# Optimization experiments

Hardware: AMD Instinct MI355X
Metric: run time of the kernel (lower is better)

Reference implementation:

```python
import jax, jax.numpy as jnp
import numpy as np

B, L, D_MODEL = 4, 2048, 1024
D_STATE, D_CONV, EXPAND, HEADDIM = 128, 4, 2, 64
D_INNER = EXPAND * D_MODEL            # 2048
NHEADS = D_INNER // HEADDIM           # 32
CONV_DIM = D_INNER + 2 * D_STATE      # 2304
D_IN_PROJ = 2 * D_INNER + 2 * D_STATE + NHEADS  # 4448
EPS = 1e-5


def _silu(v):
    return v * jax.nn.sigmoid(v)


def setup_inputs() -> dict:
    key = jax.random.key(0)
    ks = jax.random.split(key, 8)
    x = jax.random.normal(ks[0], (B, L, D_MODEL), dtype=jnp.float32)
    ln_w = jnp.ones((D_MODEL,), jnp.float32)
    ln_b = jnp.zeros((D_MODEL,), jnp.float32)
    in_proj_w = jax.random.normal(ks[1], (D_IN_PROJ, D_MODEL), jnp.float32) * 0.02
    conv_w = jax.random.normal(ks[2], (CONV_DIM, D_CONV), jnp.float32) * 0.2
    conv_b = jnp.zeros((CONV_DIM,), jnp.float32)
    # inverse-softplus of dt sampled in [1e-3, 1e-1], matching mamba2 dt init
    dt_bias = jnp.log(jnp.expm1(jax.random.uniform(ks[3], (NHEADS,), minval=0.001, maxval=0.1)))
    # A sampled uniform in [1,16], stored as log (A = -exp(A_log))
    A_log = jnp.log(jax.random.uniform(ks[4], (NHEADS,), minval=1.0, maxval=16.0))
    D = jnp.ones((NHEADS,), jnp.float32)
    rms_w = jnp.ones((D_INNER,), jnp.float32)
    out_proj_w = jax.random.normal(ks[5], (D_MODEL, D_INNER), jnp.float32) * 0.02
    return {"x": x, "ln_w": ln_w, "ln_b": ln_b, "in_proj_w": in_proj_w,
            "conv_w": conv_w, "conv_b": conv_b, "dt_bias": dt_bias,
            "A_log": A_log, "D": D, "rms_w": rms_w, "out_proj_w": out_proj_w}


def reference(x, ln_w, ln_b, in_proj_w, conv_w, conv_b, dt_bias, A_log, D, rms_w, out_proj_w):
    b = x.shape[0]
    # LayerNorm
    mu = x.mean(-1, keepdims=True)
    var = ((x - mu) ** 2).mean(-1, keepdims=True)
    u = (x - mu) * jax.lax.rsqrt(var + EPS) * ln_w + ln_b
    # input projection -> z | xBC | dt
    zxbcdt = jnp.einsum('bld,ed->ble', u, in_proj_w)
    z = zxbcdt[..., :D_INNER]
    xBC = zxbcdt[..., D_INNER:D_INNER + CONV_DIM]
    dt = jax.nn.softplus(zxbcdt[..., -NHEADS:] + dt_bias)  # (b,l,h)
    # causal depthwise conv along time (kernel D_CONV) + silu
    xpad = jnp.pad(xBC, ((0, 0), (D_CONV - 1, 0), (0, 0)))
    conv = conv_b + sum(conv_w[:, k] * xpad[:, k:k + L, :] for k in range(D_CONV))
    xBC = _silu(conv)
    xh = xBC[..., :D_INNER].reshape(b, L, NHEADS, HEADDIM)       # (b,l,h,p)
    Bm = xBC[..., D_INNER:D_INNER + D_STATE]                      # (b,l,n)
    Cm = xBC[..., D_INNER + D_STATE:]                             # (b,l,n)
    A = -jnp.exp(A_log)                                           # (h,)
    dA = jnp.exp(dt * A)                                          # (b,l,h)
    dtx = dt[..., None] * xh                                      # (b,l,h,p)

    def step(h, inp):
        dA_t, dtx_t, B_t, C_t = inp
        h = dA_t[:, :, None, None] * h + dtx_t[..., None] * B_t[:, None, None, :]
        y_t = jnp.einsum('bhpn,bn->bhp', h, C_t)
        return h, y_t

    h0 = jnp.zeros((b, NHEADS, HEADDIM, D_STATE), x.dtype)
    xs = (dA.transpose(1, 0, 2), dtx.transpose(1, 0, 2, 3),
          Bm.transpose(1, 0, 2), Cm.transpose(1, 0, 2))
    _, ys = jax.lax.scan(step, h0, xs)                            # (l,b,h,p)
    y = ys.transpose(1, 0, 2, 3) + D[None, None, :, None] * xh    # skip term
    y = y.reshape(b, L, D_INNER)
    # gated RMSNorm: rmsnorm(y * silu(z)) * weight
    g = y * _silu(z)
    g = g * jax.lax.rsqrt((g * g).mean(-1, keepdims=True) + EPS) * rms_w
    out = jnp.einsum('ble,de->bld', g, out_proj_w)
    # residual; dropout is identity in eval mode
    return out + x
```

## Files before the change

### kernel.cpp

```cpp
#include <hip/hip_runtime.h>
#include <hip/hip_bf16.h>

#define DEV __device__ __forceinline__

typedef unsigned short u16;
typedef unsigned int u32;
typedef float f32x4 __attribute__((ext_vector_type(4)));
typedef short s16x8 __attribute__((ext_vector_type(8)));

static constexpr int Bb = 4, Ll = 2048, DM = 1024, DI = 2048, NH = 32;
static constexpr int CD = 2304;
static constexpr int NP = 4384;
static constexpr int NP_PAD = 4480;
static constexpr int BL = Bb * Ll;
static constexpr int NC = 32;

DEV float u2f(u16 s) { return __uint_as_float(((u32)s) << 16); }
DEV u16 f2bu(float f) {
  __hip_bfloat16 h = __float2bfloat16(f);
  u16 s; __builtin_memcpy(&s, &h, 2); return s;
}
DEV float blo(u32 u) { return __uint_as_float(u << 16); }
DEV float bhi(u32 u) { return __uint_as_float(u & 0xffff0000u); }

DEV int swz64(int r, int k)  { return r * 64  + ((((k >> 3) ^ (r & 7))) << 3) + (k & 7); }

DEV void gl_lds16(const u16* g, u16* l) {
  __builtin_amdgcn_global_load_lds(
      (const __attribute__((address_space(1))) u32*)g,
      (__attribute__((address_space(3))) u32*)l, 16, 0, 0);
}

__global__ __launch_bounds__(256) void cvt_pad(const float* __restrict__ src,
    u16* __restrict__ dst, int total, int cols, int realRows) {
  int i = blockIdx.x * 256 + threadIdx.x;
  if (i >= total) return;
  int r = i / cols;
  dst[i] = (r < realRows) ? f2bu(src[i]) : (u16)0;
}

__global__ __launch_bounds__(256) void ln_kernel(const float* __restrict__ x,
    const float* __restrict__ w, const float* __restrict__ bia, u16* __restrict__ u) {
  int row = blockIdx.x, tid = threadIdx.x;
  const float4* xr = (const float4*)(x + (size_t)row * DM);
  float4 v = xr[tid];
  float s = v.x + v.y + v.z + v.w;
  float s2 = v.x*v.x + v.y*v.y + v.z*v.z + v.w*v.w;
  #pragma unroll
  for (int o = 32; o; o >>= 1) { s += __shfl_down(s, o); s2 += __shfl_down(s2, o); }
  __shared__ float rs[4], rs2[4];
  int wv = tid >> 6, ln = tid & 63;
  if (ln == 0) { rs[wv] = s; rs2[wv] = s2; }
  __syncthreads();
  s = rs[0] + rs[1] + rs[2] + rs[3];
  s2 = rs2[0] + rs2[1] + rs2[2] + rs2[3];
  float mu = s * (1.f / DM);
  float var = s2 * (1.f / DM) - mu * mu;
  float inv = rsqrtf(var + 1e-5f);
  float4 wv4 = ((const float4*)w)[tid], bv4 = ((const float4*)bia)[tid];
  ushort4 o;
  o.x = f2bu((v.x - mu) * inv * wv4.x + bv4.x);
  o.y = f2bu((v.y - mu) * inv * wv4.y + bv4.y);
  o.z = f2bu((v.z - mu) * inv * wv4.z + bv4.z);
  o.w = f2bu((v.w - mu) * inv * wv4.w + bv4.w);
  ((ushort4*)(u + (size_t)row * DM))[tid] = o;
}

__global__ __launch_bounds__(512, 4) void gemm_in8(const u16* __restrict__ A,
    const u16* __restrict__ Bw, u16* __restrict__ zbuf, u16* __restrict__ xbc,
    u16* __restrict__ dtraw) {
  __shared__ u16 SH[24576];
  int tid = threadIdx.x, wid = tid >> 6, lane = tid & 63;
  int fr = lane & 15, fq = lane >> 4;
  int nb = blockIdx.x;
  int xcd = nb & 7, i = nb >> 3;
  int m0 = (xcd * 4 + (i & 3)) * 256;
  int n0 = (i >> 2) * 128;
  int wm = (wid >> 1) * 64, wn = (wid & 1) * 64;
  int ksrcE = (((lane & 3) ^ ((lane >> 3) & 3)) << 3);
  int lr = lane >> 2;

  f32x4 acc[4][4];
  #pragma unroll
  for (int a = 0; a < 4; a++)
    #pragma unroll
    for (int b = 0; b < 4; b++) acc[a][b] = (f32x4){0.f, 0.f, 0.f, 0.f};

  auto STGA = [&](int t, int dstE) {
    #pragma unroll
    for (int h = 0; h < 2; h++) {
      int r0 = h * 128 + wid * 16;
      gl_lds16(A + (size_t)(m0 + r0 + lr) * 1024 + t * 32 + ksrcE, &SH[dstE + r0 * 32]);
    }
  };
  auto STGB = [&](int t, int dstE) {
    int r0 = wid * 16;
    gl_lds16(Bw + (size_t)(n0 + r0 + lr) * 1024 + t * 32 + ksrcE, &SH[dstE + r0 * 32]);
  };

  STGA(0, 0);
  STGB(0, 16384);
  asm volatile("s_waitcnt vmcnt(0)" ::: "memory");
  __builtin_amdgcn_s_barrier();
  for (int t = 0; t < 32; t++) {
    int ca = (t & 1) * 8192, cbf = 16384 + (t & 1) * 4096;
    if (t < 31) {
      STGA(t + 1, ((t + 1) & 1) * 8192);
      STGB(t + 1, 16384 + ((t + 1) & 1) * 4096);
    }
    s16x8 bB[4];
    #pragma unroll
    for (int nf = 0; nf < 4; nf++) {
      int rb = wn + nf * 16 + fr;
      bB[nf] = *(const s16x8*)&SH[cbf + rb * 32 + ((fq ^ ((rb >> 1) & 3)) << 3)];
    }
    __builtin_amdgcn_s_setprio(1);
    #pragma unroll
    for (int mf = 0; mf < 4; mf++) {
      int ra = wm + mf * 16 + fr;
      s16x8 af = *(const s16x8*)&SH[ca + ra * 32 + ((fq ^ ((ra >> 1) & 3)) << 3)];
      #pragma unroll
      for (int nf = 0; nf < 4; nf++)
        acc[mf][nf] = __builtin_amdgcn_mfma_f32_16x16x32_bf16(af, bB[nf], acc[mf][nf], 0, 0, 0);
    }
    __builtin_amdgcn_s_setprio(0);
    __syncthreads();
  }
  #pragma unroll
  for (int mf = 0; mf < 4; mf++) {
    #pragma unroll
    for (int nf = 0; nf < 4; nf++) {
      int col = n0 + wn + nf * 16 + fr;
      #pragma unroll
      for (int r = 0; r < 4; r++) {
        int row = m0 + wm + mf * 16 + fq * 4 + r;
        float v = acc[mf][nf][r];
        if (col < 2048)       zbuf[(size_t)row * 2048 + col] = f2bu(v);
        else if (col < 4352)  xbc[(size_t)row * 2304 + (col - 2048)] = f2bu(v);
        else if (col < 4384)  dtraw[(size_t)row * 32 + (col - 4352)] = f2bu(v);
      }
    }
  }
}

__global__ __launch_bounds__(256) void gemm_out(const u16* __restrict__ A,
    const u16* __restrict__ Bw, float* __restrict__ of,
    const float* __restrict__ resid, int N, int K) {
  __shared__ u16 sA[128 * 32];
  __shared__ u16 sB[128 * 32];
  int tid = threadIdx.x, wid = tid >> 6, lane = tid & 63;
  int m0 = blockIdx.x * 128, n0 = blockIdx.y * 128;
  int wm = (wid >> 1) * 64, wn = (wid & 1) * 64;
  f32x4 acc[4][4];
  #pragma unroll
  for (int i = 0; i < 4; i++)
    #pragma unroll
    for (int j = 0; j < 4; j++) acc[i][j] = (f32x4){0.f, 0.f, 0.f, 0.f};
  int rA = wid * 32 + (lane >> 2);
  int cA = (lane & 3) * 8;
  const u16* gA = A + (size_t)(m0 + rA) * K + cA;
  const u16* gB = Bw + (size_t)(n0 + rA) * K + cA;
  u16* lA0 = &sA[(wid * 2 + 0) * 512]; u16* lA1 = &sA[(wid * 2 + 1) * 512];
  u16* lB0 = &sB[(wid * 2 + 0) * 512]; u16* lB1 = &sB[(wid * 2 + 1) * 512];
  int fr = lane & 15, fk = (lane >> 4) * 8, fq = lane >> 4;
  for (int kk = 0; kk < K; kk += 32) {
    gl_lds16(gA + kk, lA0);
    gl_lds16(gA + (size_t)16 * K + kk, lA1);
    gl_lds16(gB + kk, lB0);
    gl_lds16(gB + (size_t)16 * K + kk, lB1);
    __syncthreads();
    s16x8 af[4], bfr[4];
    #pragma unroll
    for (int i = 0; i < 4; i++) af[i] = *(const s16x8*)&sA[(wm + i * 16 + fr) * 32 + fk];
    #pragma unroll
    for (int i = 0; i < 4; i++) bfr[i] = *(const s16x8*)&sB[(wn + i * 16 + fr) * 32 + fk];
    #pragma unroll
    for (int mi = 0; mi < 4; mi++)
      #pragma unroll
      for (int ni = 0; ni < 4; ni++)
        acc[mi][ni] = __builtin_amdgcn_mfma_f32_16x16x32_bf16(af[mi], bfr[ni], acc[mi][ni], 0, 0, 0);
    __syncthreads();
  }
  #pragma unroll
  for (int mi = 0; mi < 4; mi++) {
    #pragma unroll
    for (int ni = 0; ni < 4; ni++) {
      int col = n0 + wn + ni * 16 + fr;
      #pragma unroll
      for (int r = 0; r < 4; r++) {
        int row = m0 + wm + mi * 16 + fq * 4 + r;
        of[(size_t)row * N + col] = acc[mi][ni][r] + resid[(size_t)row * N + col];
      }
    }
  }
}

__global__ __launch_bounds__(256) void conv_silu(const u16* __restrict__ xbc,
    const float* __restrict__ cw, const float* __restrict__ cb, u16* __restrict__ out) {
  int i = blockIdx.x * 256 + threadIdx.x;
  if (i >= BL * (CD / 8)) return;
  int c8 = i % (CD / 8);
  int bl = i / (CD / 8);
  int l = bl & (Ll - 1);
  int c0 = c8 * 8;
  uint4 R[4];
  #pragma unroll
  for (int k = 0; k < 4; k++) {
    int ls = l - 3 + k;
    if (ls >= 0) R[k] = *(const uint4*)(xbc + (size_t)(bl - 3 + k) * CD + c0);
    else         R[k] = (uint4){0u, 0u, 0u, 0u};
  }
  u16 o[8];
  #pragma unroll
  for (int e = 0; e < 8; e++) {
    float acc = cb[c0 + e];
    float4 wv = *(const float4*)(cw + (size_t)(c0 + e) * 4);
    float wk[4] = {wv.x, wv.y, wv.z, wv.w};
    #pragma unroll
    for (int k = 0; k < 4; k++) {
      u32 word = (&R[k].x)[e >> 1];
      float xv = (e & 1) ? bhi(word) : blo(word);
      acc += wk[k] * xv;
    }
    float sg = 1.f / (1.f + __expf(-acc));
    o[e] = f2bu(acc * sg);
  }
  uint4 ov;
  ov.x = (u32)o[0] | ((u32)o[1] << 16);
  ov.y = (u32)o[2] | ((u32)o[3] << 16);
  ov.z = (u32)o[4] | ((u32)o[5] << 16);
  ov.w = (u32)o[6] | ((u32)o[7] << 16);
  *(uint4*)(out + (size_t)bl * CD + c0) = ov;
}

__global__ __launch_bounds__(256) void dt_cumsum(const u16* __restrict__ dtraw,
    const float* __restrict__ dtb, const float* __restrict__ alog,
    float* __restrict__ dtv, float* __restrict__ sv) {
  int wid = threadIdx.x >> 6, lane = threadIdx.x & 63;
  int g = blockIdx.x * 4 + wid;
  int b = g >> 10, h = (g >> 5) & 31, c = g & 31;
  int t = c * 64 + lane;
  float raw = u2f(dtraw[(size_t)(b * Ll + t) * 32 + h]);
  float v = raw + dtb[h];
  float dt = (v > 20.f) ? v : log1pf(__expf(v));
  float a = -dt * __expf(alog[h]);
  float s = a;
  #pragma unroll
  for (int o = 1; o < 64; o <<= 1) {
    float u = __shfl_up(s, o);
    if (lane >= o) s += u;
  }
  int idx = (b * 32 + h) * Ll + t;
  dtv[idx] = dt;
  sv[idx] = s;
}

__global__ __launch_bounds__(256) void chunk_state(const u16* __restrict__ conv,
    const float* __restrict__ dtv, const float* __restrict__ sv,
    u16* __restrict__ S) {
  __shared__ u16 xsT[64 * 64];
  __shared__ u16 BT[128 * 64];
  int gid = blockIdx.x;
  int c = gid & 31, h = (gid >> 5) & 31, b = gid >> 10;
  int bh = b * 32 + h;
  int tid = threadIdx.x, w = tid >> 6, lane = tid & 63;
  int fr = lane & 15, fq = lane >> 4;
  int j = tid & 63, pg = tid >> 6;
  int tb = c * 64;
  const float* svb = sv + (size_t)bh * Ll + tb;
  const float* dvb = dtv + (size_t)bh * Ll + tb;
  const u16* cvb = conv + (size_t)(b * Ll + tb) * CD;
  float s_last = svb[63];
  float wj = __expf(s_last - svb[j]) * dvb[j];
  const u16* rowp = cvb + (size_t)j * CD;
  #pragma unroll
  for (int rep = 0; rep < 2; rep++) {
    int p0 = rep * 32 + pg * 8;
    uint4 v = *(const uint4*)(rowp + h * 64 + p0);
    u32 va[4] = {v.x, v.y, v.z, v.w};
    #pragma unroll
    for (int e = 0; e < 4; e++) {
      xsT[swz64(p0 + 2 * e, j)]     = f2bu(blo(va[e]) * wj);
      xsT[swz64(p0 + 2 * e + 1, j)] = f2bu(bhi(va[e]) * wj);
    }
  }
  #pragma unroll
  for (int rep = 0; rep < 4; rep++) {
    int n0 = rep * 32 + pg * 8;
    uint4 v = *(const uint4*)(rowp + DI + n0);
    u32 va[4] = {v.x, v.y, v.z, v.w};
    #pragma unroll
    for (int e = 0; e < 4; e++) {
      BT[swz64(n0 + 2 * e, j)]     = (u16)(va[e] & 0xffffu);
      BT[swz64(n0 + 2 * e + 1, j)] = (u16)(va[e] >> 16);
    }
  }
  __syncthreads();
  f32x4 acc[4][2];
  #pragma unroll
  for (int mi = 0; mi < 4; mi++)
    #pragma unroll
    for (int ni = 0; ni < 2; ni++) acc[mi][ni] = (f32x4){0.f, 0.f, 0.f, 0.f};
  #pragma unroll
  for (int ks = 0; ks < 2; ks++) {
    int k8 = ks * 4 + fq;
    s16x8 bfv[2];
    #pragma unroll
    for (int ni = 0; ni < 2; ni++) {
      int rb = w * 32 + ni * 16 + fr;
      bfv[ni] = *(const s16x8*)&BT[rb * 64 + ((k8 ^ (rb & 7)) << 3)];
    }
    #pragma unroll
    for (int mi = 0; mi < 4; mi++) {
      int ra = mi * 16 + fr;
      s16x8 af = *(const s16x8*)&xsT[ra * 64 + ((k8 ^ (ra & 7)) << 3)];
      #pragma unroll
      for (int ni = 0; ni < 2; ni++)
        acc[mi][ni] = __builtin_amdgcn_mfma_f32_16x16x32_bf16(af, bfv[ni], acc[mi][ni], 0, 0, 0);
    }
  }
  u16* Sc = S + (size_t)gid * 8192;
  #pragma unroll
  for (int mi = 0; mi < 4; mi++) {
    #pragma unroll
    for (int ni = 0; ni < 2; ni++) {
      int p = mi * 16 + fq * 4;
      int n = w * 32 + ni * 16 + fr;
      #pragma unroll
      for (int r = 0; r < 4; r++)
        Sc[(size_t)(p + r) * 128 + n] = f2bu(acc[mi][ni][r]);
    }
  }
}

__global__ __launch_bounds__(256) void state_pass(u16* __restrict__ S,
    const float* __restrict__ sv) {
  int bh = blockIdx.x >> 3, q = blockIdx.x & 7;
  int o = q * 1024 + threadIdx.x * 4;
  const float* svb = sv + (size_t)bh * Ll;
  u16* base = S + (size_t)bh * NC * 8192 + o;
  float acc[4] = {0.f, 0.f, 0.f, 0.f};
  for (int c = 0; c < NC; c++) {
    uint2 sc = *(const uint2*)(base + (size_t)c * 8192);
    uint2 pre;
    pre.x = (u32)f2bu(acc[0]) | ((u32)f2bu(acc[1]) << 16);
    pre.y = (u32)f2bu(acc[2]) | ((u32)f2bu(acc[3]) << 16);
    *(uint2*)(base + (size_t)c * 8192) = pre;
    float E = __expf(svb[c * 64 + 63]);
    acc[0] = E * acc[0] + blo(sc.x);
    acc[1] = E * acc[1] + bhi(sc.x);
    acc[2] = E * acc[2] + blo(sc.y);
    acc[3] = E * acc[3] + bhi(sc.y);
  }
}

__global__ __launch_bounds__(256) void chunk_out(const u16* __restrict__ conv,
    const u16* __restrict__ hstart, const float* __restrict__ dtv,
    const float* __restrict__ sv, const float* __restrict__ Dp,
    u16* __restrict__ yb) {
  __shared__ u16 Ct[64 * 128];
  __shared__ u16 Bt[64 * 128];
  __shared__ u16 Hs[64 * 128];
  __shared__ u16 xT[64 * 64];
  __shared__ u16 Ml[64 * 64];
  __shared__ float svl[64], dtl[64], pexl[64];
  int gid = blockIdx.x;
  int c = gid & 31, h = (gid >> 5) & 31, b = gid >> 10;
  int tid = threadIdx.x, w = tid >> 6, lane = tid & 63;
  int fr = lane & 15, fq = lane >> 4;
  int tb = c * 64;
  const u16* cvb = conv + ((size_t)b * Ll + tb) * CD;
  const u16* hsrc = hstart + (((size_t)(b * 32 + h)) * NC + c) * 8192;
  #pragma unroll
  for (int qq = 0; qq < 4; qq++) {
    int q = w * 4 + qq;
    int i = q * 4 + (lane >> 4);
    int s = lane & 15;
    int kc = ((s ^ (i & 7)) << 3);
    gl_lds16(cvb + (size_t)i * CD + 2176 + kc, &Ct[q * 512]);
    gl_lds16(cvb + (size_t)i * CD + 2048 + kc, &Bt[q * 512]);
    gl_lds16(hsrc + (size_t)i * 128 + kc, &Hs[q * 512]);
  }
  {
    int j = tid & 63, pg = tid >> 6;
    const u16* rowp = cvb + (size_t)j * CD + h * 64;
    #pragma unroll
    for (int rep = 0; rep < 2; rep++) {
      int p0 = rep * 32 + pg * 8;
      uint4 v = *(const uint4*)(rowp + p0);
      u32 va[4] = {v.x, v.y, v.z, v.w};
      #pragma unroll
      for (int e = 0; e < 4; e++) {
        xT[swz64(p0 + 2 * e, j)]     = (u16)(va[e] & 0xffffu);
        xT[swz64(p0 + 2 * e + 1, j)] = (u16)(va[e] >> 16);
      }
    }
  }
  if (tid < 64) {
    float s = sv[(size_t)(b * 32 + h) * Ll + tb + tid];
    svl[tid] = s;
    pexl[tid] = __expf(s);
    dtl[tid] = dtv[(size_t)(b * 32 + h) * Ll + tb + tid];
  }
  __syncthreads();
  f32x4 g2[4];
  #pragma unroll
  for (int mi = 0; mi < 4; mi++) g2[mi] = (f32x4){0.f, 0.f, 0.f, 0.f};
  int wj = w * 16;
  #pragma unroll
  for (int ks = 0; ks < 4; ks++) {
    int k8 = ks * 4 + fq;
    int rb = wj + fr;
    s16x8 bf = *(const s16x8*)&Bt[rb * 128 + ((k8 ^ (rb & 7)) << 3)];
    #pragma unroll
    for (int mi = 0; mi < 4; mi++) {
      int ra = mi * 16 + fr;
      s16x8 af = *(const s16x8*)&Ct[ra * 128 + ((k8 ^ (ra & 7)) << 3)];
      g2[mi] = __builtin_amdgcn_mfma_f32_16x16x32_bf16(af, bf, g2[mi], 0, 0, 0);
    }
  }
  #pragma unroll
  for (int mi = 0; mi < 4; mi++) {
    int jj = wj + fr;
    #pragma unroll
    for (int r = 0; r < 4; r++) {
      int ii = mi * 16 + fq * 4 + r;
      float v = 0.f;
      if (jj <= ii) v = g2[mi][r] * __expf(svl[ii] - svl[jj]) * dtl[jj];
      Ml[swz64(ii, jj)] = f2bu(v);
    }
  }
  __syncthreads();
  f32x4 aY[4], a4[4];
  #pragma unroll
  for (int mi = 0; mi < 4; mi++) { aY[mi] = (f32x4){0.f, 0.f, 0.f, 0.f}; a4[mi] = (f32x4){0.f, 0.f, 0.f, 0.f}; }
  int wp = w * 16;
  #pragma unroll
  for (int ks = 0; ks < 2; ks++) {
    int k8 = ks * 4 + fq;
    int rb = wp + fr;
    s16x8 bf = *(const s16x8*)&xT[rb * 64 + ((k8 ^ (rb & 7)) << 3)];
    #pragma unroll
    for (int mi = 0; mi < 4; mi++) {
      int ra = mi * 16 + fr;
      s16x8 af = *(const s16x8*)&Ml[ra * 64 + ((k8 ^ (ra & 7)) << 3)];
      aY[mi] = __builtin_amdgcn_mfma_f32_16x16x32_bf16(af, bf, aY[mi], 0, 0, 0);
    }
  }
  #pragma unroll
  for (int ks = 0; ks < 4; ks++) {
    int k8 = ks * 4 + fq;
    int rb = wp + fr;
    s16x8 bf = *(const s16x8*)&Hs[rb * 128 + ((k8 ^ (rb & 7)) << 3)];
    #pragma unroll
    for (int mi = 0; mi < 4; mi++) {
      int ra = mi * 16 + fr;
      s16x8 af = *(const s16x8*)&Ct[ra * 128 + ((k8 ^ (ra & 7)) << 3)];
      a4[mi] = __builtin_amdgcn_mfma_f32_16x16x32_bf16(af, bf, a4[mi], 0, 0, 0);
    }
  }
  float Dh = Dp[h];
  u16* yrow = yb + ((size_t)b * Ll + tb) * DI + h * 64;
  #pragma unroll
  for (int mi = 0; mi < 4; mi++) {
    int p = wp + fr;
    #pragma unroll
    for (int r = 0; r < 4; r++) {
      int i = mi * 16 + fq * 4 + r;
      float xh = u2f(xT[swz64(p, i)]);
      yrow[(size_t)i * DI + p] = f2bu(aY[mi][r] + pexl[i] * a4[mi][r] + Dh * xh);
    }
  }
}

__global__ __launch_bounds__(256) void gate_rms(const u16* __restrict__ y,
    const u16* __restrict__ zbuf, const float* __restrict__ rw, u16* __restrict__ g) {
  int bl = blockIdx.x, tid = threadIdx.x;
  uint4 yv = ((const uint4*)(y + (size_t)bl * DI))[tid];
  uint4 zv = ((const uint4*)(zbuf + (size_t)bl * DI))[tid];
  u32 ya[4] = {yv.x, yv.y, yv.z, yv.w};
  u32 za[4] = {zv.x, zv.y, zv.z, zv.w};
  float gv[8];
  float ss = 0.f;
  #pragma unroll
  for (int jx = 0; jx < 4; jx++) {
    float y0 = blo(ya[jx]), y1 = bhi(ya[jx]);
    float z0 = blo(za[jx]), z1 = bhi(za[jx]);
    float s0 = z0 / (1.f + __expf(-z0));
    float s1 = z1 / (1.f + __expf(-z1));
    gv[jx * 2] = y0 * s0; gv[jx * 2 + 1] = y1 * s1;
    ss += gv[jx * 2] * gv[jx * 2] + gv[jx * 2 + 1] * gv[jx * 2 + 1];
  }
  #pragma unroll
  for (int o = 32; o; o >>= 1) ss += __shfl_down(ss, o);
  __shared__ float red[4];
  int wv = tid >> 6, ln = tid & 63;
  if (ln == 0) red[wv] = ss;
  __syncthreads();
  ss = red[0] + red[1] + red[2] + red[3];
  float scale = rsqrtf(ss * (1.f / DI) + 1e-5f);
  const float* rwp = rw + tid * 8;
  ushort4 o0, o1;
  o0.x = f2bu(gv[0] * scale * rwp[0]); o0.y = f2bu(gv[1] * scale * rwp[1]);
  o0.z = f2bu(gv[2] * scale * rwp[2]); o0.w = f2bu(gv[3] * scale * rwp[3]);
  o1.x = f2bu(gv[4] * scale * rwp[4]); o1.y = f2bu(gv[5] * scale * rwp[5]);
  o1.z = f2bu(gv[6] * scale * rwp[6]); o1.w = f2bu(gv[7] * scale * rwp[7]);
  ushort4* gp = (ushort4*)(g + (size_t)bl * DI + tid * 8);
  gp[0] = o0; gp[1] = o1;
}

extern "C" void kernel_launch(void* const* d_in, const int* in_sizes, int n_in,
                              void* d_out, int out_size, void* d_ws, size_t ws_size,
                              hipStream_t stream) {
  const float* x    = (const float*)d_in[0];
  const float* lnw  = (const float*)d_in[1];
  const float* lnb  = (const float*)d_in[2];
  const float* w1   = (const float*)d_in[3];
  const float* cw   = (const float*)d_in[4];
  const float* cb   = (const float*)d_in[5];
  const float* dtb  = (const float*)d_in[6];
  const float* alog = (const float*)d_in[7];
  const float* Dp   = (const float*)d_in[8];
  const float* rw   = (const float*)d_in[9];
  const float* w2   = (const float*)d_in[10];

  char* ws = (char*)d_ws;
  u16*   ub     = (u16*)(ws + 0);
  u16*   W1b    = (u16*)(ws + 16777216);
  u16*   conv   = (u16*)(ws + 0);
  u16*   zbuf   = (u16*)(ws + 37748736);
  u16*   xbc    = (u16*)(ws + 71303168);
  u16*   dtraw  = (u16*)(ws + 109051904);
  u16*   Sbuf   = (u16*)(ws + 71303168);
  u16*   gb     = (u16*)(ws + 71303168);
  float* dtv    = (float*)(ws + 138412032);
  float* sv     = (float*)(ws + 139460608);
  u16*   yb     = (u16*)(ws + 140509184);
  u16*   W2b    = (u16*)(ws + 174063616);
  if (ws_size < 178257920u) return;

  float* out = (float*)d_out;

  cvt_pad<<<(NP_PAD * 1024) / 256, 256, 0, stream>>>(w1, W1b, NP_PAD * 1024, 1024, NP);
  cvt_pad<<<(1024 * 2048) / 256, 256, 0, stream>>>(w2, W2b, 1024 * 2048, 2048, 1024);
  ln_kernel<<<BL, 256, 0, stream>>>(x, lnw, lnb, ub);
  gemm_in8<<<1120, 512, 0, stream>>>(ub, W1b, zbuf, xbc, dtraw);
  conv_silu<<<(BL * (CD / 8)) / 256, 256, 0, stream>>>(xbc, cw, cb, conv);
  dt_cumsum<<<1024, 256, 0, stream>>>(dtraw, dtb, alog, dtv, sv);
  chunk_state<<<4096, 256, 0, stream>>>(conv, dtv, sv, Sbuf);
  state_pass<<<1024, 256, 0, stream>>>(Sbuf, sv);
  chunk_out<<<4096, 256, 0, stream>>>(conv, Sbuf, dtv, sv, Dp, yb);
  gate_rms<<<BL, 256, 0, stream>>>(yb, zbuf, rw, gb);
  gemm_out<<<dim3(64, 8), 256, 0, stream>>>(gb, W2b, out, x, 1024, 2048);
}
```

Before: 338.3 us.

## Template pipelined GEMM for both projections with partial vmcnt waits

Turns the input-projection GEMM into a template shared with the output projection, which drops the older single-buffered 128x128 gemm_out kernel. The output projection now uses the 256x128 double-buffered, swizzled, 512-thread tile with an XCD-aware block mapping. The main loop now waits with vmcnt(3) plus a raw s_barrier, so prefetch loads for the next tile stay in flight during the current MFMA work. The out GEMM launches only 256 blocks, which may underfill the GPU, and the hand-written waitcnt/barrier sequence depends on exact load counts for correctness.

```diff
diff --git a/kernel.cpp b/kernel.cpp
--- a/kernel.cpp
+++ b/kernel.cpp
@@ -66,9 +66,12 @@
   ((ushort4*)(u + (size_t)row * DM))[tid] = o;
 }
 
-__global__ __launch_bounds__(512, 4) void gemm_in8(const u16* __restrict__ A,
-    const u16* __restrict__ Bw, u16* __restrict__ zbuf, u16* __restrict__ xbc,
-    u16* __restrict__ dtraw) {
+template<int MODE>
+__global__ __launch_bounds__(512, 4) void gemm2p(const u16* __restrict__ A,
+    const u16* __restrict__ Bw, void* __restrict__ o0, u16* __restrict__ xbc,
+    u16* __restrict__ dtraw, const float* __restrict__ resid) {
+  constexpr int K = (MODE == 0) ? 1024 : 2048;
+  constexpr int NT = K / 32;
   __shared__ u16 SH[24576];
   int tid = threadIdx.x, wid = tid >> 6, lane = tid & 63;
   int fr = lane & 15, fq = lane >> 4;
@@ -90,23 +93,25 @@
     #pragma unroll
     for (int h = 0; h < 2; h++) {
       int r0 = h * 128 + wid * 16;
-      gl_lds16(A + (size_t)(m0 + r0 + lr) * 1024 + t * 32 + ksrcE, &SH[dstE + r0 * 32]);
+      gl_lds16(A + (size_t)(m0 + r0 + lr) * K + t * 32 + ksrcE, &SH[dstE + r0 * 32]);
     }
   };
   auto STGB = [&](int t, int dstE) {
     int r0 = wid * 16;
-    gl_lds16(Bw + (size_t)(n0 + r0 + lr) * 1024 + t * 32 + ksrcE, &SH[dstE + r0 * 32]);
+    gl_lds16(Bw + (size_t)(n0 + r0 + lr) * K + t * 32 + ksrcE, &SH[dstE + r0 * 32]);
   };
 
   STGA(0, 0);
   STGB(0, 16384);
-  asm volatile("s_waitcnt vmcnt(0)" ::: "memory");
-  __builtin_amdgcn_s_barrier();
-  for (int t = 0; t < 32; t++) {
+  asm volatile("s_waitcnt vmcnt(0)\n\ts_barrier" ::: "memory");
+  for (int t = 0; t < NT; t++) {
     int ca = (t & 1) * 8192, cbf = 16384 + (t & 1) * 4096;
-    if (t < 31) {
+    if (t < NT - 1) {
       STGA(t + 1, ((t + 1) & 1) * 8192);
       STGB(t + 1, 16384 + ((t + 1) & 1) * 4096);
+      asm volatile("s_waitcnt vmcnt(3)\n\ts_barrier" ::: "memory");
+    } else {
+      asm volatile("s_waitcnt vmcnt(0)\n\ts_barrier" ::: "memory");
     }
     s16x8 bB[4];
     #pragma unroll
@@ -124,72 +129,37 @@
         acc[mf][nf] = __builtin_amdgcn_mfma_f32_16x16x32_bf16(af, bB[nf], acc[mf][nf], 0, 0, 0);
     }
     __builtin_amdgcn_s_setprio(0);
-    __syncthreads();
-  }
-  #pragma unroll
-  for (int mf = 0; mf < 4; mf++) {
-    #pragma unroll
-    for (int nf = 0; nf < 4; nf++) {
-      int col = n0 + wn + nf * 16 + fr;
+    asm volatile("s_barrier" ::: "memory");
+  }
+  if (MODE == 0) {
+    u16* zbuf = (u16*)o0;
+    #pragma unroll
+    for (int mf = 0; mf < 4; mf++) {
       #pragma unroll
-      for (int r = 0; r < 4; r++) {
-        int row = m0 + wm + mf * 16 + fq * 4 + r;
-        float v = acc[mf][nf][r];
-        if (col < 2048)       zbuf[(size_t)row * 2048 + col] = f2bu(v);
-        else if (col < 4352)  xbc[(size_t)row * 2304 + (col - 2048)] = f2bu(v);
-        else if (col < 4384)  dtraw[(size_t)row * 32 + (col - 4352)] = f2bu(v);
+      for (int nf = 0; nf < 4; nf++) {
+        int col = n0 + wn + nf * 16 + fr;
+        #pragma unroll
+        for (int r = 0; r < 4; r++) {
+          int row = m0 + wm + mf * 16 + fq * 4 + r;
+          float v = acc[mf][nf][r];
+          if (col < 2048)       zbuf[(size_t)row * 2048 + col] = f2bu(v);
+          else if (col < 4352)  xbc[(size_t)row * 2304 + (col - 2048)] = f2bu(v);
+          else if (col < 4384)  dtraw[(size_t)row * 32 + (col - 4352)] = f2bu(v);
+        }
       }
     }
-  }
-}
-
-__global__ __launch_bounds__(256) void gemm_out(const u16* __restrict__ A,
-    const u16* __restrict__ Bw, float* __restrict__ of,
-    const float* __restrict__ resid, int N, int K) {
-  __shared__ u16 sA[128 * 32];
-  __shared__ u16 sB[128 * 32];
-  int tid = threadIdx.x, wid = tid >> 6, lane = tid & 63;
-  int m0 = blockIdx.x * 128, n0 = blockIdx.y * 128;
-  int wm = (wid >> 1) * 64, wn = (wid & 1) * 64;
-  f32x4 acc[4][4];
-  #pragma unroll
-  for (int i = 0; i < 4; i++)
-    #pragma unroll
-    for (int j = 0; j < 4; j++) acc[i][j] = (f32x4){0.f, 0.f, 0.f, 0.f};
-  int rA = wid * 32 + (lane >> 2);
-  int cA = (lane & 3) * 8;
-  const u16* gA = A + (size_t)(m0 + rA) * K + cA;
-  const u16* gB = Bw + (size_t)(n0 + rA) * K + cA;
-  u16* lA0 = &sA[(wid * 2 + 0) * 512]; u16* lA1 = &sA[(wid * 2 + 1) * 512];
-  u16* lB0 = &sB[(wid * 2 + 0) * 512]; u16* lB1 = &sB[(wid * 2 + 1) * 512];
-  int fr = lane & 15, fk = (lane >> 4) * 8, fq = lane >> 4;
-  for (int kk = 0; kk < K; kk += 32) {
-    gl_lds16(gA + kk, lA0);
-    gl_lds16(gA + (size_t)16 * K + kk, lA1);
-    gl_lds16(gB + kk, lB0);
-    gl_lds16(gB + (size_t)16 * K + kk, lB1);
-    __syncthreads();
-    s16x8 af[4], bfr[4];
-    #pragma unroll
-    for (int i = 0; i < 4; i++) af[i] = *(const s16x8*)&sA[(wm + i * 16 + fr) * 32 + fk];
-    #pragma unroll
-    for (int i = 0; i < 4; i++) bfr[i] = *(const s16x8*)&sB[(wn + i * 16 + fr) * 32 + fk];
-    #pragma unroll
-    for (int mi = 0; mi < 4; mi++)
+  } else {
+    float* of = (float*)o0;
+    #pragma unroll
+    for (int mf = 0; mf < 4; mf++) {
       #pragma unroll
-      for (int ni = 0; ni < 4; ni++)
-        acc[mi][ni] = __builtin_amdgcn_mfma_f32_16x16x32_bf16(af[mi], bfr[ni], acc[mi][ni], 0, 0, 0);
-    __syncthreads();
-  }
-  #pragma unroll
-  for (int mi = 0; mi < 4; mi++) {
-    #pragma unroll
-    for (int ni = 0; ni < 4; ni++) {
-      int col = n0 + wn + ni * 16 + fr;
-      #pragma unroll
-      for (int r = 0; r < 4; r++) {
-        int row = m0 + wm + mi * 16 + fq * 4 + r;
-        of[(size_t)row * N + col] = acc[mi][ni][r] + resid[(size_t)row * N + col];
+      for (int nf = 0; nf < 4; nf++) {
+        int col = n0 + wn + nf * 16 + fr;
+        #pragma unroll
+        for (int r = 0; r < 4; r++) {
+          int row = m0 + wm + mf * 16 + fq * 4 + r;
+          of[(size_t)row * 1024 + col] = acc[mf][nf][r] + resid[(size_t)row * 1024 + col];
+        }
       }
     }
   }
@@ -544,12 +514,12 @@
   cvt_pad<<<(NP_PAD * 1024) / 256, 256, 0, stream>>>(w1, W1b, NP_PAD * 1024, 1024, NP);
   cvt_pad<<<(1024 * 2048) / 256, 256, 0, stream>>>(w2, W2b, 1024 * 2048, 2048, 1024);
   ln_kernel<<<BL, 256, 0, stream>>>(x, lnw, lnb, ub);
-  gemm_in8<<<1120, 512, 0, stream>>>(ub, W1b, zbuf, xbc, dtraw);
+  gemm2p<0><<<1120, 512, 0, stream>>>(ub, W1b, zbuf, xbc, dtraw, nullptr);
   conv_silu<<<(BL * (CD / 8)) / 256, 256, 0, stream>>>(xbc, cw, cb, conv);
   dt_cumsum<<<1024, 256, 0, stream>>>(dtraw, dtb, alog, dtv, sv);
   chunk_state<<<4096, 256, 0, stream>>>(conv, dtv, sv, Sbuf);
   state_pass<<<1024, 256, 0, stream>>>(Sbuf, sv);
   chunk_out<<<4096, 256, 0, stream>>>(conv, Sbuf, dtv, sv, Dp, yb);
   gate_rms<<<BL, 256, 0, stream>>>(yb, zbuf, rw, gb);
-  gemm_out<<<dim3(64, 8), 256, 0, stream>>>(gb, W2b, out, x, 1024, 2048);
-}
+  gemm2p<1><<<256, 512, 0, stream>>>(gb, W2b, out, nullptr, nullptr, x);
+}
```

After: 327.9 us. 3.1% less time.
